# Performance work log

Measured on AMD Instinct MI355X. Metric: run time of the kernel, lower is better.

The kernel has to match this reference:

```python
import jax, jax.numpy as jnp
import numpy as np

B, N, K, DIN, C = 2, 20480, 16, 32, 64  # C = 2*d_out
EPS = 1e-5


def _ln(x, g, b):
    m = jnp.mean(x, axis=-1, keepdims=True)
    v = jnp.mean((x - m) ** 2, axis=-1, keepdims=True)
    return (x - m) * jax.lax.rsqrt(v + EPS) * g + b


def _gather(pc, idx):
    # pc: (B, N, D), idx: (B, N, K) -> (B, N, K, D)
    Bq, Nq, Kq = idx.shape
    D = pc.shape[-1]
    flat = idx.reshape(Bq, Nq * Kq, 1)
    return jnp.take_along_axis(pc, flat, axis=1).reshape(Bq, Nq, Kq, D)


def setup_inputs() -> dict:
    key = jax.random.key(0)
    ks = jax.random.split(key, 40)
    rn = lambda k, s, sc=0.05: jax.random.normal(k, s, dtype=jnp.float32) * sc
    inp = {
        "feature": rn(ks[0], (B, DIN, N, 1), 1.0),
        "xyz": jax.random.uniform(ks[1], (B, N, 3), dtype=jnp.float32),
        "W1": rn(ks[2], (C, DIN)), "b1": rn(ks[3], (C,)),
        "Wq": rn(ks[4], (C, C)), "bq": rn(ks[5], (C,)),
        "Wk": rn(ks[6], (C, C)), "bk": rn(ks[7], (C,)),
        "Wv": rn(ks[8], (C, C)), "bv": rn(ks[9], (C,)),
        "Wd1": rn(ks[10], (3, 3), 0.3), "bd1": rn(ks[11], (3,)),
        "lnd1_g": 1.0 + rn(ks[12], (3,)), "lnd1_b": rn(ks[13], (3,)),
        "Wd2": rn(ks[14], (C, 3), 0.3), "bd2": rn(ks[15], (C,)),
        "Wg1": rn(ks[16], (C, C)), "bg1": rn(ks[17], (C,)),
        "lng1_g": 1.0 + rn(ks[18], (C,)), "lng1_b": rn(ks[19], (C,)),
        "Wg2": rn(ks[20], (C, C)), "bg2": rn(ks[21], (C,)),
        "lng2_g": 1.0 + rn(ks[22], (C,)), "lng2_b": rn(ks[23], (C,)),
        "Wmlp": rn(ks[24], (C, C)),
        "bnm_g": 1.0 + rn(ks[25], (C,)), "bnm_b": rn(ks[26], (C,)),
        "bnm_m": rn(ks[27], (C,)), "bnm_v": 1.0 + jax.random.uniform(ks[28], (C,), dtype=jnp.float32) * 0.1,
        "Wsc": rn(ks[29], (C, DIN)),
        "bns_g": 1.0 + rn(ks[30], (C,)), "bns_b": rn(ks[31], (C,)),
        "bns_m": rn(ks[32], (C,)), "bns_v": 1.0 + jax.random.uniform(ks[33], (C,), dtype=jnp.float32) * 0.1,
        "neigh_idx": jax.random.randint(ks[34], (B, N, K), 0, N),
    }
    return inp


def reference(feature, xyz, W1, b1, Wq, bq, Wk, bk, Wv, bv, Wd1, bd1, lnd1_g, lnd1_b,
              Wd2, bd2, Wg1, bg1, lng1_g, lng1_b, Wg2, bg2, lng2_g, lng2_b,
              Wmlp, bnm_g, bnm_b, bnm_m, bnm_v, Wsc, bns_g, bns_b, bns_m, bns_v,
              neigh_idx):
    f = jnp.transpose(feature[..., 0], (0, 2, 1))          # (B, N, DIN)
    x = f @ W1.T + b1                                      # (B, N, C)
    q = x @ Wq.T + bq                                      # (B, N, C)
    kf = _gather(x @ Wk.T + bk, neigh_idx)                 # (B, N, K, C)
    vf = _gather(x @ Wv.T + bv, neigh_idx)                 # (B, N, K, C)
    knn_xyz = _gather(xyz, neigh_idx)                      # (B, N, K, 3)
    rel = xyz[:, :, None, :] - knn_xyz                     # (B, N, K, 3)
    pos = rel @ Wd1.T + bd1
    pos = jax.nn.relu(_ln(pos, lnd1_g, lnd1_b))
    pos = pos @ Wd2.T + bd2                                # (B, N, K, C)
    attn = q[:, :, None, :] - kf + pos
    attn = jax.nn.relu(_ln(attn, lng1_g, lng1_b)) @ Wg1.T + bg1
    attn = jax.nn.relu(_ln(attn, lng2_g, lng2_b)) @ Wg2.T + bg2
    attn = jax.nn.softmax(attn, axis=2)                    # softmax over K
    res = jnp.sum(attn * (vf + pos), axis=2)               # (B, N, C)
    # mlp: 1x1 conv (no bias) + BN(eval) + ReLU
    res = res @ Wmlp.T
    res = jax.nn.relu(bnm_g * (res - bnm_m) * jax.lax.rsqrt(bnm_v + EPS) + bnm_b)
    # shortcut: 1x1 conv (no bias) + BN(eval) + ReLU
    sc = f @ Wsc.T
    sc = jax.nn.relu(bns_g * (sc - bns_m) * jax.lax.rsqrt(bns_v + EPS) + bns_b)
    out = jax.nn.leaky_relu(res + sc, negative_slope=0.2)  # (B, N, C)
    return jnp.transpose(out, (0, 2, 1))[..., None]        # (B, C, N, 1)
```

## Files before the change

### kernel.cpp

```cpp
#include <hip/hip_runtime.h>

#define N_ 20480
#define EPS_ 1e-5f

typedef __bf16 bf16;
typedef __attribute__((ext_vector_type(8))) __bf16 bf16x8;
typedef __attribute__((ext_vector_type(4))) __bf16 bf16x4;
typedef __attribute__((ext_vector_type(4))) float f32x4;
typedef __attribute__((ext_vector_type(2))) float f32x2;

#define WS_WG1   0
#define WS_WG2   8192
#define WS_PCST  16384
#define WS_L1    17408
#define WS_L2    17920
#define WS_BG1   18432
#define WS_BG2   18688
#define WS_WQ    18944
#define WS_WK    23040
#define WS_WV    27136
#define WS_WSC   31232
#define WS_WMLP  35328
#define WS_BQ    43520
#define WS_BK    43776
#define WS_BV    44032
#define WS_BSC   44288
#define WS_BMLP  44544
#define WS_PD1   44800
#define WS_FLAG  44872
#define WS_PREP  45056

template <typename T>
__device__ __forceinline__ float ldf(const T* p, size_t i) { return (float)p[i]; }

__device__ __forceinline__ int sniff_dtype(const unsigned int* xyz_raw) {
  const int t = threadIdx.x;
  __shared__ int cnt[256];
  int local = 0;
  for (int i = t; i < 4096; i += 256) {
    unsigned int wv = xyz_raw[i];
    unsigned int b1 = (wv >> 8) & 0xFFu;
    local += (b1 >= 0x30u && b1 < 0x45u) ? 1 : 0;
  }
  cnt[t] = local;
  __syncthreads();
  for (int s = 128; s > 0; s >>= 1) {
    if (t < s) cnt[t] += cnt[t + s];
    __syncthreads();
  }
  int r = (cnt[0] > 2048) ? 1 : 0;
  __syncthreads();
  return r;
}

template <typename T>
__device__ void prep_body(const T* W1, const T* b1, const T* Wq, const T* bq,
                          const T* Wk, const T* bk, const T* Wv, const T* bv,
                          const T* Wd1, const T* bd1, const T* lnd1_g, const T* lnd1_b,
                          const T* Wd2, const T* bd2,
                          const T* Wg1, const T* bg1, const T* lng1_g, const T* lng1_b,
                          const T* Wg2, const T* bg2, const T* lng2_g, const T* lng2_b,
                          const T* Wmlp, const T* bnm_g, const T* bnm_b, const T* bnm_m, const T* bnm_v,
                          const T* Wsc, const T* bns_g, const T* bns_b, const T* bns_m, const T* bns_v,
                          char* wsp) {
  const int tid = blockIdx.x * 256 + threadIdx.x;
  const int T_ = gridDim.x * 256;
  bf16* wg1bf = (bf16*)(wsp + WS_WG1);
  bf16* wg2bf = (bf16*)(wsp + WS_WG2);
  bf16* wmlpbf = (bf16*)(wsp + WS_WMLP);
  bf16* wscbf = (bf16*)(wsp + WS_WSC);
  bf16* wqbf = (bf16*)(wsp + WS_WQ);
  bf16* wkbf = (bf16*)(wsp + WS_WK);
  bf16* wvbf = (bf16*)(wsp + WS_WV);
  float* pcst = (float*)(wsp + WS_PCST);
  float* l1c = (float*)(wsp + WS_L1);
  float* l2c = (float*)(wsp + WS_L2);
  float* bg1f = (float*)(wsp + WS_BG1);
  float* bg2f = (float*)(wsp + WS_BG2);
  float* bqf = (float*)(wsp + WS_BQ);
  float* bkf = (float*)(wsp + WS_BK);
  float* bvf = (float*)(wsp + WS_BV);
  float* bscf = (float*)(wsp + WS_BSC);
  float* bmlpf = (float*)(wsp + WS_BMLP);
  float* pd1 = (float*)(wsp + WS_PD1);

  for (int i = tid; i < 4096; i += T_) {
// ... 102 lines not shown

  bf16x8 fa;
  #pragma unroll
  for (int j = 0; j < 8; ++j)
    fa[j] = (__bf16)ldf(feat, ((size_t)b * 32 + g * 8 + j) * N_ + n0 + m);

  auto matmul16 = [&](const bf16* wbf, const float* bias, float* ob) {
    #pragma unroll
    for (int tt = 0; tt < 4; ++tt) {
      bf16x8 wf = *(const bf16x8*)(wbf + (tt * 16 + m) * 32 + g * 8);
      float bb = bias[tt * 16 + m];
      f32x4 ci = {bb, bb, bb, bb};
      ci = __builtin_amdgcn_mfma_f32_16x16x32_bf16(fa, wf, ci, 0, 0, 0);
      #pragma unroll
      for (int r = 0; r < 4; ++r) tw[g * 4 + r][tt * 16 + m] = ci[r];
    }
    #pragma unroll
    for (int s = 0; s < 2; ++s) {
      f32x4 v0 = *(f32x4*)&tw[m][s * 32 + g * 8];
      f32x4 v1 = *(f32x4*)&tw[m][s * 32 + g * 8 + 4];
      #pragma unroll
      for (int r = 0; r < 4; ++r) { ob[s * 8 + r] = v0[r]; ob[s * 8 + 4 + r] = v1[r]; }
    }
  };
  float ob[16];
  bf16x8 o0, o1;
  matmul16(wqbf, bqf, ob);
  #pragma unroll
  for (int j = 0; j < 8; ++j) { o0[j] = (__bf16)ob[j]; o1[j] = (__bf16)ob[8 + j]; }
  *(bf16x8*)(q_ws + (size_t)(p0 + m) * 64 + g * 8) = o0;
  *(bf16x8*)(q_ws + (size_t)(p0 + m) * 64 + 32 + g * 8) = o1;
  matmul16(wkbf, bkf, ob);
  #pragma unroll
  for (int j = 0; j < 8; ++j) { o0[j] = (__bf16)ob[j]; o1[j] = (__bf16)ob[8 + j]; }
  *(bf16x8*)(k_ws + (size_t)(p0 + m) * 64 + g * 8) = o0;
  *(bf16x8*)(k_ws + (size_t)(p0 + m) * 64 + 32 + g * 8) = o1;
  matmul16(wvbf, bvf, ob);
  #pragma unroll
  for (int j = 0; j < 8; ++j) { o0[j] = (__bf16)ob[j]; o1[j] = (__bf16)ob[8 + j]; }
  *(bf16x8*)(v_ws + (size_t)(p0 + m) * 64 + g * 8) = o0;
  *(bf16x8*)(v_ws + (size_t)(p0 + m) * 64 + 32 + g * 8) = o1;
}

__launch_bounds__(256)
__global__ void xqkv_kernel(const void* feat, char* wsp,
                            bf16* q_ws, bf16* k_ws, bf16* v_ws) {
  __shared__ float tile[64][68];
  const int* flag = (const int*)(wsp + WS_FLAG);
  if (flag[0]) xqkv_body<bf16>((const bf16*)feat, wsp, q_ws, k_ws, v_ws, tile);
  else         xqkv_body<float>((const float*)feat, wsp, q_ws, k_ws, v_ws, tile);
}

template <typename T>
__device__ void attn_body(const T* xyz, const int* nidx, const char* wsp,
                          bf16* qres, const bf16* k_ws, const bf16* v_ws,
                          f32x4* pcstL, f32x2* l1L, f32x2* l2L,
                          bf16 (*vpf)[72], bf16 (*scr)[72]) {
  const int t = threadIdx.x;
  ((float*)pcstL)[t] = ((const float*)(wsp + WS_PCST))[t];
  if (t < 128) ((float*)l1L)[t] = ((const float*)(wsp + WS_L1))[t];
  else if (t < 256) ((float*)l2L)[t - 128] = ((const float*)(wsp + WS_L2))[t - 128];
  __syncthreads();

  const int w = t >> 6, lane = t & 63, m = lane & 15, g = lane >> 4;
  const int p = blockIdx.x * 4 + w;
  const int b = p / N_;
  bf16 (*vw)[72] = vpf + w * 16;
  bf16 (*sw)[72] = scr + w * 16;

  const float* pd1 = (const float*)(wsp + WS_PD1);
  const float* bg1f = (const float*)(wsp + WS_BG1);
  const float* bg2f = (const float*)(wsp + WS_BG2);
  const bf16* wg1bf = (const bf16*)(wsp + WS_WG1);
  const bf16* wg2bf = (const bf16*)(wsp + WS_WG2);

  float bg1r[4], bg2r[4];
  #pragma unroll
  for (int tt = 0; tt < 4; ++tt) { bg1r[tt] = bg1f[tt * 16 + m]; bg2r[tt] = bg2f[tt * 16 + m]; }

  float xp = ldf(xyz, (size_t)p * 3 + 0);
  float yp = ldf(xyz, (size_t)p * 3 + 1);
  float zp = ldf(xyz, (size_t)p * 3 + 2);

  int idx = nidx[(size_t)p * 16 + m];
  size_t pg = (size_t)b * N_ + idx;
  bf16x8 kf0 = *(const bf16x8*)(k_ws + pg * 64 + g * 8);
  bf16x8 kf1 = *(const bf16x8*)(k_ws + pg * 64 + 32 + g * 8);
  bf16x8 vf0 = *(const bf16x8*)(v_ws + pg * 64 + g * 8);
  bf16x8 vf1 = *(const bf16x8*)(v_ws + pg * 64 + 32 + g * 8);
  bf16x8 qf0 = *(const bf16x8*)(qres + (size_t)p * 64 + g * 8);
  bf16x8 qf1 = *(const bf16x8*)(qres + (size_t)p * 64 + 32 + g * 8);
  float nx = ldf(xyz, pg * 3 + 0), ny = ldf(xyz, pg * 3 + 1), nz = ldf(xyz, pg * 3 + 2);

  float rx = xp - nx, ry = yp - ny, rz = zp - nz;
  float pp0 = pd1[0] * rx + pd1[1] * ry + pd1[2] * rz + pd1[9];
  float pp1 = pd1[3] * rx + pd1[4] * ry + pd1[5] * rz + pd1[10];
  float pp2 = pd1[6] * rx + pd1[7] * ry + pd1[8] * rz + pd1[11];
  float mu3 = (pp0 + pp1 + pp2) * (1.f / 3.f);
  float q0 = pp0 - mu3, q1 = pp1 - mu3, q2 = pp2 - mu3;
  float vr3 = (q0 * q0 + q1 * q1 + q2 * q2) * (1.f / 3.f);
  float rs3 = rsqrtf(vr3 + EPS_);
  float h0 = fmaxf(q0 * rs3 * pd1[12] + pd1[15], 0.f);
  float h1 = fmaxf(q1 * rs3 * pd1[13] + pd1[16], 0.f);
  float h2 = fmaxf(q2 * rs3 * pd1[14] + pd1[17], 0.f);

  float a[16];
  #pragma unroll
  for (int s = 0; s < 2; ++s)
    #pragma unroll
    for (int half = 0; half < 2; ++half) {
      bf16x4 vb;
      #pragma unroll
      for (int q4 = 0; q4 < 4; ++q4) {
        int j = half * 4 + q4;
        int c = s * 32 + g * 8 + j;
        f32x4 pc = pcstL[c];
        float pos = fmaf(h0, pc[0], fmaf(h1, pc[1], fmaf(h2, pc[2], pc[3])));
        float kv = (float)((s == 0) ? kf0[j] : kf1[j]);
        float vv = (float)((s == 0) ? vf0[j] : vf1[j]);
        float qv = (float)((s == 0) ? qf0[j] : qf1[j]);
        vb[q4] = (__bf16)(vv + pos);
        a[s * 8 + j] = qv - kv + pos;
      }
      *(bf16x4*)&vw[m][s * 32 + g * 8 + half * 4] = vb;
    }

  f32x4 acc[4];
  bf16x8 hf0, hf1;

  {
    float s1 = 0.f, s2 = 0.f;
    #pragma unroll
    for (int i = 0; i < 16; ++i) { s1 += a[i]; s2 = fmaf(a[i], a[i], s2); }
    s1 += __shfl_xor(s1, 16); s2 += __shfl_xor(s2, 16);
    s1 += __shfl_xor(s1, 32); s2 += __shfl_xor(s2, 32);
    float mean = s1 * (1.f / 64.f);
    float var = s2 * (1.f / 64.f) - mean * mean;
    float rsv = rsqrtf(var + EPS_);
    #pragma unroll
    for (int s = 0; s < 2; ++s)
      #pragma unroll
      for (int j = 0; j < 8; ++j) {
        int c = s * 32 + g * 8 + j;
        f32x2 lc = l1L[c];
        float hh = fmaxf(fmaf((a[s * 8 + j] - mean) * rsv, lc[0], lc[1]), 0.f);
        if (s == 0) hf0[j] = (__bf16)hh; else hf1[j] = (__bf16)hh;
      }
  }
  #pragma unroll
  for (int tt = 0; tt < 4; ++tt) {
    bf16x8 w0 = *(const bf16x8*)(wg1bf + (tt * 16 + m) * 64 + g * 8);
    bf16x8 w1 = *(const bf16x8*)(wg1bf + (tt * 16 + m) * 64 + 32 + g * 8);
    f32x4 ci = {bg1r[tt], bg1r[tt], bg1r[tt], bg1r[tt]};
    ci = __builtin_amdgcn_mfma_f32_16x16x32_bf16(hf0, w0, ci, 0, 0, 0);
    ci = __builtin_amdgcn_mfma_f32_16x16x32_bf16(hf1, w1, ci, 0, 0, 0);
    acc[tt] = ci;
  }
  #pragma unroll
  for (int tt = 0; tt < 4; ++tt)
    #pragma unroll
    for (int r = 0; r < 4; ++r)
      sw[g * 4 + r][tt * 16 + m] = (__bf16)acc[tt][r];
  #pragma unroll
  for (int s = 0; s < 2; ++s) {
    bf16x8 av = *(bf16x8*)&sw[m][s * 32 + g * 8];
    #pragma unroll
    for (int j = 0; j < 8; ++j) a[s * 8 + j] = (float)av[j];
  }
  {
    float s1 = 0.f, s2 = 0.f;
    #pragma unroll
    for (int i = 0; i < 16; ++i) { s1 += a[i]; s2 = fmaf(a[i], a[i], s2); }
    s1 += __shfl_xor(s1, 16); s2 += __shfl_xor(s2, 16);
    s1 += __shfl_xor(s1, 32); s2 += __shfl_xor(s2, 32);
    float mean = s1 * (1.f / 64.f);
    float var = s2 * (1.f / 64.f) - mean * mean;
    float rsv = rsqrtf(var + EPS_);
    #pragma unroll
    for (int s = 0; s < 2; ++s)
      #pragma unroll
      for (int j = 0; j < 8; ++j) {
        int c = s * 32 + g * 8 + j;
        f32x2 lc = l2L[c];
        float hh = fmaxf(fmaf((a[s * 8 + j] - mean) * rsv, lc[0], lc[1]), 0.f);
        if (s == 0) hf0[j] = (__bf16)hh; else hf1[j] = (__bf16)hh;
      }
  }
  #pragma unroll
  for (int tt = 0; tt < 4; ++tt) {
    bf16x8 w0 = *(const bf16x8*)(wg2bf + (tt * 16 + m) * 64 + g * 8);
    bf16x8 w1 = *(const bf16x8*)(wg2bf + (tt * 16 + m) * 64 + 32 + g * 8);
    f32x4 ci = {bg2r[tt], bg2r[tt], bg2r[tt], bg2r[tt]};
    ci = __builtin_amdgcn_mfma_f32_16x16x32_bf16(hf0, w0, ci, 0, 0, 0);
    ci = __builtin_amdgcn_mfma_f32_16x16x32_bf16(hf1, w1, ci, 0, 0, 0);
    acc[tt] = ci;
  }
  float resv[4];
  #pragma unroll
  for (int tt = 0; tt < 4; ++tt) {
    f32x4 l = acc[tt];
    float mx = fmaxf(fmaxf(l[0], l[1]), fmaxf(l[2], l[3]));
    mx = fmaxf(mx, __shfl_xor(mx, 16));
    mx = fmaxf(mx, __shfl_xor(mx, 32));
    float x0 = __expf(l[0] - mx), x1 = __expf(l[1] - mx);
    float x2 = __expf(l[2] - mx), x3 = __expf(l[3] - mx);
    float ss = x0 + x1 + x2 + x3;
    ss += __shfl_xor(ss, 16); ss += __shfl_xor(ss, 32);
    int cc = tt * 16 + m;
    float part = x0 * (float)vw[g * 4 + 0][cc] + x1 * (float)vw[g * 4 + 1][cc]
               + x2 * (float)vw[g * 4 + 2][cc] + x3 * (float)vw[g * 4 + 3][cc];
    part += __shfl_xor(part, 16); part += __shfl_xor(part, 32);
    resv[tt] = part / ss;
  }
  float outv = (g == 0) ? resv[0] : (g == 1) ? resv[1] : (g == 2) ? resv[2] : resv[3];
  qres[(size_t)p * 64 + lane] = (__bf16)outv;
}

__launch_bounds__(256)
__global__ void attn_kernel(const void* xyz, const int* __restrict__ nidx, char* wsp,
                            bf16* qres, const bf16* k_ws, const bf16* v_ws) {
  __shared__ f32x4 pcstL[64];
  __shared__ f32x2 l1L[64];
  __shared__ f32x2 l2L[64];
  __shared__ bf16 vpf[64][72];
  __shared__ bf16 scr[64][72];
  const int* flag = (const int*)(wsp + WS_FLAG);
  if (flag[0])
    attn_body<bf16>((const bf16*)xyz, nidx, wsp, qres, k_ws, v_ws, pcstL, l1L, l2L, vpf, scr);
  else
    attn_body<float>((const float*)xyz, nidx, wsp, qres, k_ws, v_ws, pcstL, l1L, l2L, vpf, scr);
}

template <typename T>
__device__ void out_body(const T* feat, const bf16* res_ws, const char* wsp, T* out,
                         float (*tileT)[69]) {
  const int t = threadIdx.x, w = t >> 6, lane = t & 63;
  const int m = lane & 15, g = lane >> 4;
  const int p0blk = blockIdx.x * 64;
  const int b = p0blk / N_, n0 = p0blk % N_;
  const int p0w = p0blk + w * 16;
  const bf16* wmlpbf = (const bf16*)(wsp + WS_WMLP);
  const bf16* wscbf = (const bf16*)(wsp + WS_WSC);
  const float* bmlpf = (const float*)(wsp + WS_BMLP);
  const float* bscf = (const float*)(wsp + WS_BSC);

  bf16x8 ar0 = *(const bf16x8*)(res_ws + (size_t)(p0w + m) * 64 + g * 8);
  bf16x8 ar1 = *(const bf16x8*)(res_ws + (size_t)(p0w + m) * 64 + 32 + g * 8);
  bf16x8 af;
  #pragma unroll
  for (int j = 0; j < 8; ++j)
    af[j] = (__bf16)ldf(feat, ((size_t)b * 32 + g * 8 + j) * N_ + (n0 + w * 16) + m);

  #pragma unroll
  for (int tt = 0; tt < 4; ++tt) {
    bf16x8 wm0 = *(const bf16x8*)(wmlpbf + (tt * 16 + m) * 64 + g * 8);
    bf16x8 wm1 = *(const bf16x8*)(wmlpbf + (tt * 16 + m) * 64 + 32 + g * 8);
    bf16x8 wsf = *(const bf16x8*)(wscbf + (tt * 16 + m) * 32 + g * 8);
    float bm = bmlpf[tt * 16 + m], bs = bscf[tt * 16 + m];
    f32x4 cm = {bm, bm, bm, bm};
    cm = __builtin_amdgcn_mfma_f32_16x16x32_bf16(ar0, wm0, cm, 0, 0, 0);
    cm = __builtin_amdgcn_mfma_f32_16x16x32_bf16(ar1, wm1, cm, 0, 0, 0);
    f32x4 cs = {bs, bs, bs, bs};
    cs = __builtin_amdgcn_mfma_f32_16x16x32_bf16(af, wsf, cs, 0, 0, 0);
    #pragma unroll
    for (int r = 0; r < 4; ++r) {
      float o = fmaxf(cm[r], 0.f) + fmaxf(cs[r], 0.f);
      o = (o > 0.f) ? o : 0.2f * o;
      tileT[tt * 16 + m][w * 16 + g * 4 + r] = o;
    }
  }
  __syncthreads();
  const int ln = t & 63, grp = t >> 6;
  #pragma unroll
  for (int k = 0; k < 16; ++k) {
    int c2 = grp * 16 + k;
    out[((size_t)b * 64 + c2) * N_ + n0 + ln] = (T)tileT[c2][ln];
  }
}

__launch_bounds__(256)
__global__ void out_kernel(const void* feat, const bf16* res_ws, char* wsp, void* out) {
  __shared__ float tileT[64][69];
  const int* flag = (const int*)(wsp + WS_FLAG);
  if (flag[0]) out_body<bf16>((const bf16*)feat, res_ws, wsp, (bf16*)out, tileT);
  else         out_body<float>((const float*)feat, res_ws, wsp, (float*)out, tileT);
}

extern "C" void kernel_launch(void* const* d_in, const int* in_sizes, int n_in,
                              void* d_out, int out_size, void* d_ws, size_t ws_size,
                              hipStream_t stream) {
  const void* feature = d_in[0];
  const void* xyz     = d_in[1];
  const int*  nidx    = (const int*)d_in[34];

  char* ws = (char*)d_ws;
  bf16* q_ws = (bf16*)(ws + WS_PREP);
  bf16* k_ws = (bf16*)(ws + WS_PREP + 5242880);
  bf16* v_ws = (bf16*)(ws + WS_PREP + 10485760);

  prep_kernel<<<64, 256, 0, stream>>>(xyz,
                                      d_in[2], d_in[3], d_in[4], d_in[5], d_in[6], d_in[7],
                                      d_in[8], d_in[9], d_in[10], d_in[11], d_in[12], d_in[13],
                                      d_in[14], d_in[15], d_in[16], d_in[17], d_in[18], d_in[19],
                                      d_in[20], d_in[21], d_in[22], d_in[23], d_in[24], d_in[25],
                                      d_in[26], d_in[27], d_in[28], d_in[29], d_in[30], d_in[31],
                                      d_in[32], d_in[33], ws);
  xqkv_kernel<<<640, 256, 0, stream>>>(feature, ws, q_ws, k_ws, v_ws);
  attn_kernel<<<10240, 256, 0, stream>>>(xyz, nidx, ws, q_ws, k_ws, v_ws);
  out_kernel<<<640, 256, 0, stream>>>(feature, q_ws, ws, d_out);
}
```

Measured before the change: 268.3 us.

## Fuse output MLP and shortcut into attention kernel, 16 points per block

Folds the output projection, shortcut conv, BN-ReLU and leaky ReLU into the attention kernel. Each block now handles 16 points, four per wave over a loop, and keeps the attention result in shared memory. This removes one kernel launch and the workspace round trip of the intermediate result. In exchange there are four times fewer blocks, a serial per-wave loop, and output stores of 4-element chunks instead of fully coalesced 64-wide rows.

```diff
diff --git a/kernel.cpp b/kernel.cpp
--- a/kernel.cpp
+++ b/kernel.cpp
@@ -8,6 +8,7 @@
 typedef __attribute__((ext_vector_type(4))) __bf16 bf16x4;
 typedef __attribute__((ext_vector_type(4))) float f32x4;
 typedef __attribute__((ext_vector_type(2))) float f32x2;
+typedef __attribute__((ext_vector_type(4))) unsigned short u16x4;
 
 #define WS_WG1   0
 #define WS_WG2   8192
@@ -32,6 +33,23 @@
 
 template <typename T>
 __device__ __forceinline__ float ldf(const T* p, size_t i) { return (float)p[i]; }
+
+__device__ __forceinline__ unsigned short f2bfu(float f) {
+  union { __bf16 b; unsigned short u; } cv; cv.b = (__bf16)f; return cv.u;
+}
+
+template <typename T>
+__device__ __forceinline__ void store4(T* p, float a, float b, float c, float d);
+template <>
+__device__ __forceinline__ void store4<bf16>(bf16* p, float a, float b, float c, float d) {
+  u16x4 v = {f2bfu(a), f2bfu(b), f2bfu(c), f2bfu(d)};
+  *(u16x4*)p = v;
+}
+template <>
+__device__ __forceinline__ void store4<float>(float* p, float a, float b, float c, float d) {
+  f32x4 v = {a, b, c, d};
+  *(f32x4*)p = v;
+}
 
 __device__ __forceinline__ int sniff_dtype(const unsigned int* xyz_raw) {
   const int t = threadIdx.x;
@@ -240,10 +258,10 @@
 }
 
 template <typename T>
-__device__ void attn_body(const T* xyz, const int* nidx, const char* wsp,
-                          bf16* qres, const bf16* k_ws, const bf16* v_ws,
+__device__ void attn_body(const T* xyz, const T* feat, const int* nidx, const char* wsp,
+                          const bf16* q_ws, const bf16* k_ws, const bf16* v_ws, T* out,
                           f32x4* pcstL, f32x2* l1L, f32x2* l2L,
-                          bf16 (*vpf)[72], bf16 (*scr)[72]) {
+                          bf16 (*vpf)[72], bf16 (*scr)[72], bf16 (*res_tile)[72]) {
   const int t = threadIdx.x;
   ((float*)pcstL)[t] = ((const float*)(wsp + WS_PCST))[t];
   if (t < 128) ((float*)l1L)[t] = ((const float*)(wsp + WS_L1))[t];
@@ -251,8 +269,8 @@
   __syncthreads();
 
   const int w = t >> 6, lane = t & 63, m = lane & 15, g = lane >> 4;
-  const int p = blockIdx.x * 4 + w;
-  const int b = p / N_;
+  const int p0 = blockIdx.x * 16;
+  const int b = p0 / N_, n0 = p0 % N_;
   bf16 (*vw)[72] = vpf + w * 16;
   bf16 (*sw)[72] = scr + w * 16;
 
@@ -266,212 +284,198 @@
   #pragma unroll
   for (int tt = 0; tt < 4; ++tt) { bg1r[tt] = bg1f[tt * 16 + m]; bg2r[tt] = bg2f[tt * 16 + m]; }
 
-  float xp = ldf(xyz, (size_t)p * 3 + 0);
-  float yp = ldf(xyz, (size_t)p * 3 + 1);
-  float zp = ldf(xyz, (size_t)p * 3 + 2);
-
-  int idx = nidx[(size_t)p * 16 + m];
-  size_t pg = (size_t)b * N_ + idx;
-  bf16x8 kf0 = *(const bf16x8*)(k_ws + pg * 64 + g * 8);
-  bf16x8 kf1 = *(const bf16x8*)(k_ws + pg * 64 + 32 + g * 8);
-  bf16x8 vf0 = *(const bf16x8*)(v_ws + pg * 64 + g * 8);
-  bf16x8 vf1 = *(const bf16x8*)(v_ws + pg * 64 + 32 + g * 8);
-  bf16x8 qf0 = *(const bf16x8*)(qres + (size_t)p * 64 + g * 8);
-  bf16x8 qf1 = *(const bf16x8*)(qres + (size_t)p * 64 + 32 + g * 8);
-  float nx = ldf(xyz, pg * 3 + 0), ny = ldf(xyz, pg * 3 + 1), nz = ldf(xyz, pg * 3 + 2);
-
-  float rx = xp - nx, ry = yp - ny, rz = zp - nz;
-  float pp0 = pd1[0] * rx + pd1[1] * ry + pd1[2] * rz + pd1[9];
-  float pp1 = pd1[3] * rx + pd1[4] * ry + pd1[5] * rz + pd1[10];
-  float pp2 = pd1[6] * rx + pd1[7] * ry + pd1[8] * rz + pd1[11];
-  float mu3 = (pp0 + pp1 + pp2) * (1.f / 3.f);
-  float q0 = pp0 - mu3, q1 = pp1 - mu3, q2 = pp2 - mu3;
-  float vr3 = (q0 * q0 + q1 * q1 + q2 * q2) * (1.f / 3.f);
-  float rs3 = rsqrtf(vr3 + EPS_);
-  float h0 = fmaxf(q0 * rs3 * pd1[12] + pd1[15], 0.f);
-  float h1 = fmaxf(q1 * rs3 * pd1[13] + pd1[16], 0.f);
-  float h2 = fmaxf(q2 * rs3 * pd1[14] + pd1[17], 0.f);
-
-  float a[16];
-  #pragma unroll
-  for (int s = 0; s < 2; ++s)
-    #pragma unroll
-    for (int half = 0; half < 2; ++half) {
-      bf16x4 vb;
-      #pragma unroll
-      for (int q4 = 0; q4 < 4; ++q4) {
-        int j = half * 4 + q4;
-        int c = s * 32 + g * 8 + j;
-        f32x4 pc = pcstL[c];
-        float pos = fmaf(h0, pc[0], fmaf(h1, pc[1], fmaf(h2, pc[2], pc[3])));
-        float kv = (float)((s == 0) ? kf0[j] : kf1[j]);
-        float vv = (float)((s == 0) ? vf0[j] : vf1[j]);
-        float qv = (float)((s == 0) ? qf0[j] : qf1[j]);
-        vb[q4] = (__bf16)(vv + pos);
-        a[s * 8 + j] = qv - kv + pos;
+  bf16x8 af;
+  #pragma unroll
+  for (int j = 0; j < 8; ++j)
+    af[j] = (__bf16)ldf(feat, ((size_t)b * 32 + g * 8 + j) * N_ + n0 + m);
+
+  #pragma unroll 1
+  for (int it = 0; it < 4; ++it) {
+    const int ptl = w * 4 + it;
+    const int p = p0 + ptl;
+
+    float xp = ldf(xyz, (size_t)p * 3 + 0);
+    float yp = ldf(xyz, (size_t)p * 3 + 1);
+    float zp = ldf(xyz, (size_t)p * 3 + 2);
+
+    int idx = nidx[(size_t)p * 16 + m];
+    size_t pg = (size_t)b * N_ + idx;
+    bf16x8 kf0 = *(const bf16x8*)(k_ws + pg * 64 + g * 8);
+    bf16x8 kf1 = *(const bf16x8*)(k_ws + pg * 64 + 32 + g * 8);
+    bf16x8 vf0 = *(const bf16x8*)(v_ws + pg * 64 + g * 8);
+    bf16x8 vf1 = *(const bf16x8*)(v_ws + pg * 64 + 32 + g * 8);
+    bf16x8 qf0 = *(const bf16x8*)(q_ws + (size_t)p * 64 + g * 8);
+    bf16x8 qf1 = *(const bf16x8*)(q_ws + (size_t)p * 64 + 32 + g * 8);
+    float nx = ldf(xyz, pg * 3 + 0), ny = ldf(xyz, pg * 3 + 1), nz = ldf(xyz, pg * 3 + 2);
+
+    float rx = xp - nx, ry = yp - ny, rz = zp - nz;
+    float pp0 = pd1[0] * rx + pd1[1] * ry + pd1[2] * rz + pd1[9];
+    float pp1 = pd1[3] * rx + pd1[4] * ry + pd1[5] * rz + pd1[10];
+    float pp2 = pd1[6] * rx + pd1[7] * ry + pd1[8] * rz + pd1[11];
+    float mu3 = (pp0 + pp1 + pp2) * (1.f / 3.f);
+    float q0 = pp0 - mu3, q1 = pp1 - mu3, q2 = pp2 - mu3;
+    float vr3 = (q0 * q0 + q1 * q1 + q2 * q2) * (1.f / 3.f);
+    float rs3 = rsqrtf(vr3 + EPS_);
+    float h0 = fmaxf(q0 * rs3 * pd1[12] + pd1[15], 0.f);
+    float h1 = fmaxf(q1 * rs3 * pd1[13] + pd1[16], 0.f);
+    float h2 = fmaxf(q2 * rs3 * pd1[14] + pd1[17], 0.f);
+
+    float a[16];
+    #pragma unroll
+    for (int s = 0; s < 2; ++s)
+      #pragma unroll
+      for (int half = 0; half < 2; ++half) {
+        bf16x4 vb;
+        #pragma unroll
+        for (int q4 = 0; q4 < 4; ++q4) {
+          int j = half * 4 + q4;
+          int c = s * 32 + g * 8 + j;
+          f32x4 pc = pcstL[c];
+          float pos = fmaf(h0, pc[0], fmaf(h1, pc[1], fmaf(h2, pc[2], pc[3])));
+          float kv = (float)((s == 0) ? kf0[j] : kf1[j]);
+          float vv = (float)((s == 0) ? vf0[j] : vf1[j]);
+          float qv = (float)((s == 0) ? qf0[j] : qf1[j]);
+          vb[q4] = (__bf16)(vv + pos);
+          a[s * 8 + j] = qv - kv + pos;
+        }
+        *(bf16x4*)&vw[m][s * 32 + g * 8 + half * 4] = vb;
       }
-      *(bf16x4*)&vw[m][s * 32 + g * 8 + half * 4] = vb;
-    }
-
-  f32x4 acc[4];
-  bf16x8 hf0, hf1;
-
-  {
-    float s1 = 0.f, s2 = 0.f;
-    #pragma unroll
-    for (int i = 0; i < 16; ++i) { s1 += a[i]; s2 = fmaf(a[i], a[i], s2); }
-    s1 += __shfl_xor(s1, 16); s2 += __shfl_xor(s2, 16);
-    s1 += __shfl_xor(s1, 32); s2 += __shfl_xor(s2, 32);
-    float mean = s1 * (1.f / 64.f);
-    float var = s2 * (1.f / 64.f) - mean * mean;
-    float rsv = rsqrtf(var + EPS_);
-    #pragma unroll
-    for (int s = 0; s < 2; ++s)
-      #pragma unroll
-      for (int j = 0; j < 8; ++j) {
-        int c = s * 32 + g * 8 + j;
-        f32x2 lc = l1L[c];
-        float hh = fmaxf(fmaf((a[s * 8 + j] - mean) * rsv, lc[0], lc[1]), 0.f);
-        if (s == 0) hf0[j] = (__bf16)hh; else hf1[j] = (__bf16)hh;
-      }
-  }
-  #pragma unroll
-  for (int tt = 0; tt < 4; ++tt) {
-    bf16x8 w0 = *(const bf16x8*)(wg1bf + (tt * 16 + m) * 64 + g * 8);
-    bf16x8 w1 = *(const bf16x8*)(wg1bf + (tt * 16 + m) * 64 + 32 + g * 8);
-    f32x4 ci = {bg1r[tt], bg1r[tt], bg1r[tt], bg1r[tt]};
-    ci = __builtin_amdgcn_mfma_f32_16x16x32_bf16(hf0, w0, ci, 0, 0, 0);
-    ci = __builtin_amdgcn_mfma_f32_16x16x32_bf16(hf1, w1, ci, 0, 0, 0);
-    acc[tt] = ci;
-  }
-  #pragma unroll
-  for (int tt = 0; tt < 4; ++tt)
-    #pragma unroll
-    for (int r = 0; r < 4; ++r)
-      sw[g * 4 + r][tt * 16 + m] = (__bf16)acc[tt][r];
-  #pragma unroll
-  for (int s = 0; s < 2; ++s) {
-    bf16x8 av = *(bf16x8*)&sw[m][s * 32 + g * 8];
-    #pragma unroll
-    for (int j = 0; j < 8; ++j) a[s * 8 + j] = (float)av[j];
-  }
-  {
-    float s1 = 0.f, s2 = 0.f;
-    #pragma unroll
-    for (int i = 0; i < 16; ++i) { s1 += a[i]; s2 = fmaf(a[i], a[i], s2); }
-    s1 += __shfl_xor(s1, 16); s2 += __shfl_xor(s2, 16);
-    s1 += __shfl_xor(s1, 32); s2 += __shfl_xor(s2, 32);
-    float mean = s1 * (1.f / 64.f);
-    float var = s2 * (1.f / 64.f) - mean * mean;
-    float rsv = rsqrtf(var + EPS_);
-    #pragma unroll
-    for (int s = 0; s < 2; ++s)
-      #pragma unroll
-      for (int j = 0; j < 8; ++j) {
-        int c = s * 32 + g * 8 + j;
-        f32x2 lc = l2L[c];
-        float hh = fmaxf(fmaf((a[s * 8 + j] - mean) * rsv, lc[0], lc[1]), 0.f);
-        if (s == 0) hf0[j] = (__bf16)hh; else hf1[j] = (__bf16)hh;
-      }
-  }
-  #pragma unroll
-  for (int tt = 0; tt < 4; ++tt) {
-    bf16x8 w0 = *(const bf16x8*)(wg2bf + (tt * 16 + m) * 64 + g * 8);
-    bf16x8 w1 = *(const bf16x8*)(wg2bf + (tt * 16 + m) * 64 + 32 + g * 8);
-    f32x4 ci = {bg2r[tt], bg2r[tt], bg2r[tt], bg2r[tt]};
-    ci = __builtin_amdgcn_mfma_f32_16x16x32_bf16(hf0, w0, ci, 0, 0, 0);
-    ci = __builtin_amdgcn_mfma_f32_16x16x32_bf16(hf1, w1, ci, 0, 0, 0);
-    acc[tt] = ci;
-  }
-  float resv[4];
-  #pragma unroll
-  for (int tt = 0; tt < 4; ++tt) {
-    f32x4 l = acc[tt];
-    float mx = fmaxf(fmaxf(l[0], l[1]), fmaxf(l[2], l[3]));
-    mx = fmaxf(mx, __shfl_xor(mx, 16));
-    mx = fmaxf(mx, __shfl_xor(mx, 32));
-    float x0 = __expf(l[0] - mx), x1 = __expf(l[1] - mx);
-    float x2 = __expf(l[2] - mx), x3 = __expf(l[3] - mx);
-    float ss = x0 + x1 + x2 + x3;
-    ss += __shfl_xor(ss, 16); ss += __shfl_xor(ss, 32);
-    int cc = tt * 16 + m;
-    float part = x0 * (float)vw[g * 4 + 0][cc] + x1 * (float)vw[g * 4 + 1][cc]
-               + x2 * (float)vw[g * 4 + 2][cc] + x3 * (float)vw[g * 4 + 3][cc];
-    part += __shfl_xor(part, 16); part += __shfl_xor(part, 32);
-    resv[tt] = part / ss;
-  }
-  float outv = (g == 0) ? resv[0] : (g == 1) ? resv[1] : (g == 2) ? resv[2] : resv[3];
-  qres[(size_t)p * 64 + lane] = (__bf16)outv;
+
+    f32x4 acc[4];
+    bf16x8 hf0, hf1;
+
+    {
+      float s1 = 0.f, s2 = 0.f;
+      #pragma unroll
+      for (int i = 0; i < 16; ++i) { s1 += a[i]; s2 = fmaf(a[i], a[i], s2); }
+      s1 += __shfl_xor(s1, 16); s2 += __shfl_xor(s2, 16);
+      s1 += __shfl_xor(s1, 32); s2 += __shfl_xor(s2, 32);
+      float mean = s1 * (1.f / 64.f);
+      float var = s2 * (1.f / 64.f) - mean * mean;
+      float rsv = rsqrtf(var + EPS_);
+      #pragma unroll
+      for (int s = 0; s < 2; ++s)
+        #pragma unroll
+        for (int j = 0; j < 8; ++j) {
+          int c = s * 32 + g * 8 + j;
+          f32x2 lc = l1L[c];
+          float hh = fmaxf(fmaf((a[s * 8 + j] - mean) * rsv, lc[0], lc[1]), 0.f);
+          if (s == 0) hf0[j] = (__bf16)hh; else hf1[j] = (__bf16)hh;
+        }
+    }
+    #pragma unroll
+    for (int tt = 0; tt < 4; ++tt) {
+      bf16x8 w0 = *(const bf16x8*)(wg1bf + (tt * 16 + m) * 64 + g * 8);
+      bf16x8 w1 = *(const bf16x8*)(wg1bf + (tt * 16 + m) * 64 + 32 + g * 8);
+      f32x4 ci = {bg1r[tt], bg1r[tt], bg1r[tt], bg1r[tt]};
+      ci = __builtin_amdgcn_mfma_f32_16x16x32_bf16(hf0, w0, ci, 0, 0, 0);
+      ci = __builtin_amdgcn_mfma_f32_16x16x32_bf16(hf1, w1, ci, 0, 0, 0);
+      acc[tt] = ci;
+    }
+    #pragma unroll
+    for (int tt = 0; tt < 4; ++tt)
+      #pragma unroll
+      for (int r = 0; r < 4; ++r)
+        sw[g * 4 + r][tt * 16 + m] = (__bf16)acc[tt][r];
+    #pragma unroll
+    for (int s = 0; s < 2; ++s) {
+      bf16x8 av = *(bf16x8*)&sw[m][s * 32 + g * 8];
+      #pragma unroll
+      for (int j = 0; j < 8; ++j) a[s * 8 + j] = (float)av[j];
+    }
+    {
+      float s1 = 0.f, s2 = 0.f;
+      #pragma unroll
+      for (int i = 0; i < 16; ++i) { s1 += a[i]; s2 = fmaf(a[i], a[i], s2); }
+      s1 += __shfl_xor(s1, 16); s2 += __shfl_xor(s2, 16);
+      s1 += __shfl_xor(s1, 32); s2 += __shfl_xor(s2, 32);
+      float mean = s1 * (1.f / 64.f);
+      float var = s2 * (1.f / 64.f) - mean * mean;
+      float rsv = rsqrtf(var + EPS_);
+      #pragma unroll
+      for (int s = 0; s < 2; ++s)
+        #pragma unroll
+        for (int j = 0; j < 8; ++j) {
+          int c = s * 32 + g * 8 + j;
+          f32x2 lc = l2L[c];
+          float hh = fmaxf(fmaf((a[s * 8 + j] - mean) * rsv, lc[0], lc[1]), 0.f);
+          if (s == 0) hf0[j] = (__bf16)hh; else hf1[j] = (__bf16)hh;
+        }
+    }
+    #pragma unroll
+    for (int tt = 0; tt < 4; ++tt) {
+      bf16x8 w0 = *(const bf16x8*)(wg2bf + (tt * 16 + m) * 64 + g * 8);
+      bf16x8 w1 = *(const bf16x8*)(wg2bf + (tt * 16 + m) * 64 + 32 + g * 8);
+      f32x4 ci = {bg2r[tt], bg2r[tt], bg2r[tt], bg2r[tt]};
+      ci = __builtin_amdgcn_mfma_f32_16x16x32_bf16(hf0, w0, ci, 0, 0, 0);
+      ci = __builtin_amdgcn_mfma_f32_16x16x32_bf16(hf1, w1, ci, 0, 0, 0);
+      acc[tt] = ci;
+    }
+    float resv[4];
+    #pragma unroll
+    for (int tt = 0; tt < 4; ++tt) {
+      f32x4 l = acc[tt];
+      float mx = fmaxf(fmaxf(l[0], l[1]), fmaxf(l[2], l[3]));
+      mx = fmaxf(mx, __shfl_xor(mx, 16));
+      mx = fmaxf(mx, __shfl_xor(mx, 32));
+      float x0 = __expf(l[0] - mx), x1 = __expf(l[1] - mx);
+      float x2 = __expf(l[2] - mx), x3 = __expf(l[3] - mx);
+      float ss = x0 + x1 + x2 + x3;
+      ss += __shfl_xor(ss, 16); ss += __shfl_xor(ss, 32);
+      int cc = tt * 16 + m;
+      float part = x0 * (float)vw[g * 4 + 0][cc] + x1 * (float)vw[g * 4 + 1][cc]
+                 + x2 * (float)vw[g * 4 + 2][cc] + x3 * (float)vw[g * 4 + 3][cc];
+      part += __shfl_xor(part, 16); part += __shfl_xor(part, 32);
+      resv[tt] = part / ss;
+    }
+    float outv = (g == 0) ? resv[0] : (g == 1) ? resv[1] : (g == 2) ? resv[2] : resv[3];
+    res_tile[ptl][lane] = (__bf16)outv;
+  }
+
+  __syncthreads();
+
+  const bf16* wmlpbf = (const bf16*)(wsp + WS_WMLP);
+  const bf16* wscbf = (const bf16*)(wsp + WS_WSC);
+  const float* bmlpf = (const float*)(wsp + WS_BMLP);
+  const float* bscf = (const float*)(wsp + WS_BSC);
+
+  bf16x8 ar0 = *(const bf16x8*)&res_tile[m][g * 8];
+  bf16x8 ar1 = *(const bf16x8*)&res_tile[m][32 + g * 8];
+  bf16x8 wm0 = *(const bf16x8*)(wmlpbf + (w * 16 + m) * 64 + g * 8);
+  bf16x8 wm1 = *(const bf16x8*)(wmlpbf + (w * 16 + m) * 64 + 32 + g * 8);
+  bf16x8 wsf = *(const bf16x8*)(wscbf + (w * 16 + m) * 32 + g * 8);
+  float bm = bmlpf[w * 16 + m], bs = bscf[w * 16 + m];
+  f32x4 cm = {bm, bm, bm, bm};
+  cm = __builtin_amdgcn_mfma_f32_16x16x32_bf16(ar0, wm0, cm, 0, 0, 0);
+  cm = __builtin_amdgcn_mfma_f32_16x16x32_bf16(ar1, wm1, cm, 0, 0, 0);
+  f32x4 cs = {bs, bs, bs, bs};
+  cs = __builtin_amdgcn_mfma_f32_16x16x32_bf16(af, wsf, cs, 0, 0, 0);
+  float o[4];
+  #pragma unroll
+  for (int r = 0; r < 4; ++r) {
+    float v = fmaxf(cm[r], 0.f) + fmaxf(cs[r], 0.f);
+    o[r] = (v > 0.f) ? v : 0.2f * v;
+  }
+  store4(out + ((size_t)b * 64 + w * 16 + m) * N_ + n0 + g * 4, o[0], o[1], o[2], o[3]);
 }
 
 __launch_bounds__(256)
-__global__ void attn_kernel(const void* xyz, const int* __restrict__ nidx, char* wsp,
-                            bf16* qres, const bf16* k_ws, const bf16* v_ws) {
+__global__ void attn_kernel(const void* xyz, const void* feat, const int* __restrict__ nidx,
+                            char* wsp, const bf16* q_ws, const bf16* k_ws, const bf16* v_ws,
+                            void* out) {
   __shared__ f32x4 pcstL[64];
   __shared__ f32x2 l1L[64];
   __shared__ f32x2 l2L[64];
   __shared__ bf16 vpf[64][72];
   __shared__ bf16 scr[64][72];
+  __shared__ bf16 res_tile[16][72];
   const int* flag = (const int*)(wsp + WS_FLAG);
   if (flag[0])
-    attn_body<bf16>((const bf16*)xyz, nidx, wsp, qres, k_ws, v_ws, pcstL, l1L, l2L, vpf, scr);
+    attn_body<bf16>((const bf16*)xyz, (const bf16*)feat, nidx, wsp, q_ws, k_ws, v_ws,
+                    (bf16*)out, pcstL, l1L, l2L, vpf, scr, res_tile);
   else
-    attn_body<float>((const float*)xyz, nidx, wsp, qres, k_ws, v_ws, pcstL, l1L, l2L, vpf, scr);
-}
-
-template <typename T>
-__device__ void out_body(const T* feat, const bf16* res_ws, const char* wsp, T* out,
-                         float (*tileT)[69]) {
-  const int t = threadIdx.x, w = t >> 6, lane = t & 63;
-  const int m = lane & 15, g = lane >> 4;
-  const int p0blk = blockIdx.x * 64;
-  const int b = p0blk / N_, n0 = p0blk % N_;
-  const int p0w = p0blk + w * 16;
-  const bf16* wmlpbf = (const bf16*)(wsp + WS_WMLP);
-  const bf16* wscbf = (const bf16*)(wsp + WS_WSC);
-  const float* bmlpf = (const float*)(wsp + WS_BMLP);
-  const float* bscf = (const float*)(wsp + WS_BSC);
-
-  bf16x8 ar0 = *(const bf16x8*)(res_ws + (size_t)(p0w + m) * 64 + g * 8);
-  bf16x8 ar1 = *(const bf16x8*)(res_ws + (size_t)(p0w + m) * 64 + 32 + g * 8);
-  bf16x8 af;
-  #pragma unroll
-  for (int j = 0; j < 8; ++j)
-    af[j] = (__bf16)ldf(feat, ((size_t)b * 32 + g * 8 + j) * N_ + (n0 + w * 16) + m);
-
-  #pragma unroll
-  for (int tt = 0; tt < 4; ++tt) {
-    bf16x8 wm0 = *(const bf16x8*)(wmlpbf + (tt * 16 + m) * 64 + g * 8);
-    bf16x8 wm1 = *(const bf16x8*)(wmlpbf + (tt * 16 + m) * 64 + 32 + g * 8);
-    bf16x8 wsf = *(const bf16x8*)(wscbf + (tt * 16 + m) * 32 + g * 8);
-    float bm = bmlpf[tt * 16 + m], bs = bscf[tt * 16 + m];
-    f32x4 cm = {bm, bm, bm, bm};
-    cm = __builtin_amdgcn_mfma_f32_16x16x32_bf16(ar0, wm0, cm, 0, 0, 0);
-    cm = __builtin_amdgcn_mfma_f32_16x16x32_bf16(ar1, wm1, cm, 0, 0, 0);
-    f32x4 cs = {bs, bs, bs, bs};
-    cs = __builtin_amdgcn_mfma_f32_16x16x32_bf16(af, wsf, cs, 0, 0, 0);
-    #pragma unroll
-    for (int r = 0; r < 4; ++r) {
-      float o = fmaxf(cm[r], 0.f) + fmaxf(cs[r], 0.f);
-      o = (o > 0.f) ? o : 0.2f * o;
-      tileT[tt * 16 + m][w * 16 + g * 4 + r] = o;
-    }
-  }
-  __syncthreads();
-  const int ln = t & 63, grp = t >> 6;
-  #pragma unroll
-  for (int k = 0; k < 16; ++k) {
-    int c2 = grp * 16 + k;
-    out[((size_t)b * 64 + c2) * N_ + n0 + ln] = (T)tileT[c2][ln];
-  }
-}
-
-__launch_bounds__(256)
-__global__ void out_kernel(const void* feat, const bf16* res_ws, char* wsp, void* out) {
-  __shared__ float tileT[64][69];
-  const int* flag = (const int*)(wsp + WS_FLAG);
-  if (flag[0]) out_body<bf16>((const bf16*)feat, res_ws, wsp, (bf16*)out, tileT);
-  else         out_body<float>((const float*)feat, res_ws, wsp, (float*)out, tileT);
+    attn_body<float>((const float*)xyz, (const float*)feat, nidx, wsp, q_ws, k_ws, v_ws,
+                     (float*)out, pcstL, l1L, l2L, vpf, scr, res_tile);
 }
 
 extern "C" void kernel_launch(void* const* d_in, const int* in_sizes, int n_in,
@@ -494,6 +498,5 @@
                                       d_in[26], d_in[27], d_in[28], d_in[29], d_in[30], d_in[31],
                                       d_in[32], d_in[33], ws);
   xqkv_kernel<<<640, 256, 0, stream>>>(feature, ws, q_ws, k_ws, v_ws);
-  attn_kernel<<<10240, 256, 0, stream>>>(xyz, nidx, ws, q_ws, k_ws, v_ws);
-  out_kernel<<<640, 256, 0, stream>>>(feature, q_ws, ws, d_out);
-}
+  attn_kernel<<<2560, 256, 0, stream>>>(xyz, feature, nidx, ws, q_ws, k_ws, v_ws, d_out);
+}
```

After: 315.5 us. 17.6% more time.

## Process two points per wavefront in attention kernel to reuse weight fragments

Applied to the files above, without the earlier changes.

Each wavefront now handles two query points instead of one, so the Wg1/Wg2 weight fragments loaded per tile are shared by two sets of MFMAs. The two points' gathers and MFMAs are interleaved, which gives more independent work per wave to hide latency. The grid is halved and LDS scratch doubled. In exchange, register pressure and LDS use per block rise, which may lower occupancy.

```diff
diff --git a/kernel.cpp b/kernel.cpp
--- a/kernel.cpp
+++ b/kernel.cpp
@@ -251,10 +251,7 @@
   __syncthreads();
 
   const int w = t >> 6, lane = t & 63, m = lane & 15, g = lane >> 4;
-  const int p = blockIdx.x * 4 + w;
-  const int b = p / N_;
-  bf16 (*vw)[72] = vpf + w * 16;
-  bf16 (*sw)[72] = scr + w * 16;
+  const int pbase = blockIdx.x * 8 + w * 2;
 
   const float* pd1 = (const float*)(wsp + WS_PD1);
   const float* bg1f = (const float*)(wsp + WS_BG1);
@@ -266,60 +263,69 @@
   #pragma unroll
   for (int tt = 0; tt < 4; ++tt) { bg1r[tt] = bg1f[tt * 16 + m]; bg2r[tt] = bg2f[tt * 16 + m]; }
 
-  float xp = ldf(xyz, (size_t)p * 3 + 0);
-  float yp = ldf(xyz, (size_t)p * 3 + 1);
-  float zp = ldf(xyz, (size_t)p * 3 + 2);
-
-  int idx = nidx[(size_t)p * 16 + m];
-  size_t pg = (size_t)b * N_ + idx;
-  bf16x8 kf0 = *(const bf16x8*)(k_ws + pg * 64 + g * 8);
-  bf16x8 kf1 = *(const bf16x8*)(k_ws + pg * 64 + 32 + g * 8);
-  bf16x8 vf0 = *(const bf16x8*)(v_ws + pg * 64 + g * 8);
-  bf16x8 vf1 = *(const bf16x8*)(v_ws + pg * 64 + 32 + g * 8);
-  bf16x8 qf0 = *(const bf16x8*)(qres + (size_t)p * 64 + g * 8);
-  bf16x8 qf1 = *(const bf16x8*)(qres + (size_t)p * 64 + 32 + g * 8);
-  float nx = ldf(xyz, pg * 3 + 0), ny = ldf(xyz, pg * 3 + 1), nz = ldf(xyz, pg * 3 + 2);
-
-  float rx = xp - nx, ry = yp - ny, rz = zp - nz;
-  float pp0 = pd1[0] * rx + pd1[1] * ry + pd1[2] * rz + pd1[9];
-  float pp1 = pd1[3] * rx + pd1[4] * ry + pd1[5] * rz + pd1[10];
-  float pp2 = pd1[6] * rx + pd1[7] * ry + pd1[8] * rz + pd1[11];
-  float mu3 = (pp0 + pp1 + pp2) * (1.f / 3.f);
-  float q0 = pp0 - mu3, q1 = pp1 - mu3, q2 = pp2 - mu3;
-  float vr3 = (q0 * q0 + q1 * q1 + q2 * q2) * (1.f / 3.f);
-  float rs3 = rsqrtf(vr3 + EPS_);
-  float h0 = fmaxf(q0 * rs3 * pd1[12] + pd1[15], 0.f);
-  float h1 = fmaxf(q1 * rs3 * pd1[13] + pd1[16], 0.f);
-  float h2 = fmaxf(q2 * rs3 * pd1[14] + pd1[17], 0.f);
-
-  float a[16];
-  #pragma unroll
-  for (int s = 0; s < 2; ++s)
-    #pragma unroll
-    for (int half = 0; half < 2; ++half) {
-      bf16x4 vb;
-      #pragma unroll
-      for (int q4 = 0; q4 < 4; ++q4) {
-        int j = half * 4 + q4;
-        int c = s * 32 + g * 8 + j;
-        f32x4 pc = pcstL[c];
-        float pos = fmaf(h0, pc[0], fmaf(h1, pc[1], fmaf(h2, pc[2], pc[3])));
-        float kv = (float)((s == 0) ? kf0[j] : kf1[j]);
-        float vv = (float)((s == 0) ? vf0[j] : vf1[j]);
-        float qv = (float)((s == 0) ? qf0[j] : qf1[j]);
-        vb[q4] = (__bf16)(vv + pos);
-        a[s * 8 + j] = qv - kv + pos;
+  float a[2][16];
+
+  #pragma unroll
+  for (int P = 0; P < 2; ++P) {
+    const int p = pbase + P;
+    const int b = p / N_;
+    bf16 (*vw)[72] = vpf + (w * 2 + P) * 16;
+
+    float xp = ldf(xyz, (size_t)p * 3 + 0);
+    float yp = ldf(xyz, (size_t)p * 3 + 1);
+    float zp = ldf(xyz, (size_t)p * 3 + 2);
+
+    int idx = nidx[(size_t)p * 16 + m];
+    size_t pg = (size_t)b * N_ + idx;
+    bf16x8 kf0 = *(const bf16x8*)(k_ws + pg * 64 + g * 8);
+    bf16x8 kf1 = *(const bf16x8*)(k_ws + pg * 64 + 32 + g * 8);
+    bf16x8 vf0 = *(const bf16x8*)(v_ws + pg * 64 + g * 8);
+    bf16x8 vf1 = *(const bf16x8*)(v_ws + pg * 64 + 32 + g * 8);
+    bf16x8 qf0 = *(const bf16x8*)(qres + (size_t)p * 64 + g * 8);
+    bf16x8 qf1 = *(const bf16x8*)(qres + (size_t)p * 64 + 32 + g * 8);
+    float nx = ldf(xyz, pg * 3 + 0), ny = ldf(xyz, pg * 3 + 1), nz = ldf(xyz, pg * 3 + 2);
+
+    float rx = xp - nx, ry = yp - ny, rz = zp - nz;
+    float pp0 = pd1[0] * rx + pd1[1] * ry + pd1[2] * rz + pd1[9];
+    float pp1 = pd1[3] * rx + pd1[4] * ry + pd1[5] * rz + pd1[10];
+    float pp2 = pd1[6] * rx + pd1[7] * ry + pd1[8] * rz + pd1[11];
+    float mu3 = (pp0 + pp1 + pp2) * (1.f / 3.f);
+    float q0 = pp0 - mu3, q1 = pp1 - mu3, q2 = pp2 - mu3;
+    float vr3 = (q0 * q0 + q1 * q1 + q2 * q2) * (1.f / 3.f);
+    float rs3 = rsqrtf(vr3 + EPS_);
+    float h0 = fmaxf(q0 * rs3 * pd1[12] + pd1[15], 0.f);
+    float h1 = fmaxf(q1 * rs3 * pd1[13] + pd1[16], 0.f);
+    float h2 = fmaxf(q2 * rs3 * pd1[14] + pd1[17], 0.f);
+
+    #pragma unroll
+    for (int s = 0; s < 2; ++s)
+      #pragma unroll
+      for (int half = 0; half < 2; ++half) {
+        bf16x4 vb;
+        #pragma unroll
+        for (int q4 = 0; q4 < 4; ++q4) {
+          int j = half * 4 + q4;
+          int c = s * 32 + g * 8 + j;
+          f32x4 pc = pcstL[c];
+          float pos = fmaf(h0, pc[0], fmaf(h1, pc[1], fmaf(h2, pc[2], pc[3])));
+          float kv = (float)((s == 0) ? kf0[j] : kf1[j]);
+          float vv = (float)((s == 0) ? vf0[j] : vf1[j]);
+          float qv = (float)((s == 0) ? qf0[j] : qf1[j]);
+          vb[q4] = (__bf16)(vv + pos);
+          a[P][s * 8 + j] = qv - kv + pos;
+        }
+        *(bf16x4*)&vw[m][s * 32 + g * 8 + half * 4] = vb;
       }
-      *(bf16x4*)&vw[m][s * 32 + g * 8 + half * 4] = vb;
-    }
-
-  f32x4 acc[4];
-  bf16x8 hf0, hf1;
-
-  {
+  }
+
+  bf16x8 hf0[2], hf1[2];
+  f32x4 acc[2][4];
+
+  #pragma unroll
+  for (int P = 0; P < 2; ++P) {
     float s1 = 0.f, s2 = 0.f;
     #pragma unroll
-    for (int i = 0; i < 16; ++i) { s1 += a[i]; s2 = fmaf(a[i], a[i], s2); }
+    for (int i = 0; i < 16; ++i) { s1 += a[P][i]; s2 = fmaf(a[P][i], a[P][i], s2); }
     s1 += __shfl_xor(s1, 16); s2 += __shfl_xor(s2, 16);
     s1 += __shfl_xor(s1, 32); s2 += __shfl_xor(s2, 32);
     float mean = s1 * (1.f / 64.f);
@@ -331,34 +337,46 @@
       for (int j = 0; j < 8; ++j) {
         int c = s * 32 + g * 8 + j;
         f32x2 lc = l1L[c];
-        float hh = fmaxf(fmaf((a[s * 8 + j] - mean) * rsv, lc[0], lc[1]), 0.f);
-        if (s == 0) hf0[j] = (__bf16)hh; else hf1[j] = (__bf16)hh;
+        float hh = fmaxf(fmaf((a[P][s * 8 + j] - mean) * rsv, lc[0], lc[1]), 0.f);
+        if (s == 0) hf0[P][j] = (__bf16)hh; else hf1[P][j] = (__bf16)hh;
       }
   }
   #pragma unroll
   for (int tt = 0; tt < 4; ++tt) {
     bf16x8 w0 = *(const bf16x8*)(wg1bf + (tt * 16 + m) * 64 + g * 8);
     bf16x8 w1 = *(const bf16x8*)(wg1bf + (tt * 16 + m) * 64 + 32 + g * 8);
-    f32x4 ci = {bg1r[tt], bg1r[tt], bg1r[tt], bg1r[tt]};
-    ci = __builtin_amdgcn_mfma_f32_16x16x32_bf16(hf0, w0, ci, 0, 0, 0);
-    ci = __builtin_amdgcn_mfma_f32_16x16x32_bf16(hf1, w1, ci, 0, 0, 0);
-    acc[tt] = ci;
-  }
-  #pragma unroll
-  for (int tt = 0; tt < 4; ++tt)
-    #pragma unroll
-    for (int r = 0; r < 4; ++r)
-      sw[g * 4 + r][tt * 16 + m] = (__bf16)acc[tt][r];
-  #pragma unroll
-  for (int s = 0; s < 2; ++s) {
-    bf16x8 av = *(bf16x8*)&sw[m][s * 32 + g * 8];
-    #pragma unroll
-    for (int j = 0; j < 8; ++j) a[s * 8 + j] = (float)av[j];
-  }
-  {
+    #pragma unroll
+    for (int P = 0; P < 2; ++P) {
+      f32x4 ci = {bg1r[tt], bg1r[tt], bg1r[tt], bg1r[tt]};
+      ci = __builtin_amdgcn_mfma_f32_16x16x32_bf16(hf0[P], w0, ci, 0, 0, 0);
+      ci = __builtin_amdgcn_mfma_f32_16x16x32_bf16(hf1[P], w1, ci, 0, 0, 0);
+      acc[P][tt] = ci;
+    }
+  }
+  #pragma unroll
+  for (int P = 0; P < 2; ++P) {
+    bf16 (*sw)[72] = scr + (w * 2 + P) * 16;
+    #pragma unroll
+    for (int tt = 0; tt < 4; ++tt)
+      #pragma unroll
+      for (int r = 0; r < 4; ++r)
+        sw[g * 4 + r][tt * 16 + m] = (__bf16)acc[P][tt][r];
+  }
+  #pragma unroll
+  for (int P = 0; P < 2; ++P) {
+    bf16 (*sw)[72] = scr + (w * 2 + P) * 16;
+    #pragma unroll
+    for (int s = 0; s < 2; ++s) {
+      bf16x8 av = *(bf16x8*)&sw[m][s * 32 + g * 8];
+      #pragma unroll
+      for (int j = 0; j < 8; ++j) a[P][s * 8 + j] = (float)av[j];
+    }
+  }
+  #pragma unroll
+  for (int P = 0; P < 2; ++P) {
     float s1 = 0.f, s2 = 0.f;
     #pragma unroll
-    for (int i = 0; i < 16; ++i) { s1 += a[i]; s2 = fmaf(a[i], a[i], s2); }
+    for (int i = 0; i < 16; ++i) { s1 += a[P][i]; s2 = fmaf(a[P][i], a[P][i], s2); }
     s1 += __shfl_xor(s1, 16); s2 += __shfl_xor(s2, 16);
     s1 += __shfl_xor(s1, 32); s2 += __shfl_xor(s2, 32);
     float mean = s1 * (1.f / 64.f);
@@ -370,38 +388,46 @@
       for (int j = 0; j < 8; ++j) {
         int c = s * 32 + g * 8 + j;
         f32x2 lc = l2L[c];
-        float hh = fmaxf(fmaf((a[s * 8 + j] - mean) * rsv, lc[0], lc[1]), 0.f);
-        if (s == 0) hf0[j] = (__bf16)hh; else hf1[j] = (__bf16)hh;
+        float hh = fmaxf(fmaf((a[P][s * 8 + j] - mean) * rsv, lc[0], lc[1]), 0.f);
+        if (s == 0) hf0[P][j] = (__bf16)hh; else hf1[P][j] = (__bf16)hh;
       }
   }
   #pragma unroll
   for (int tt = 0; tt < 4; ++tt) {
     bf16x8 w0 = *(const bf16x8*)(wg2bf + (tt * 16 + m) * 64 + g * 8);
     bf16x8 w1 = *(const bf16x8*)(wg2bf + (tt * 16 + m) * 64 + 32 + g * 8);
-    f32x4 ci = {bg2r[tt], bg2r[tt], bg2r[tt], bg2r[tt]};
-    ci = __builtin_amdgcn_mfma_f32_16x16x32_bf16(hf0, w0, ci, 0, 0, 0);
-    ci = __builtin_amdgcn_mfma_f32_16x16x32_bf16(hf1, w1, ci, 0, 0, 0);
-    acc[tt] = ci;
-  }
-  float resv[4];
-  #pragma unroll
-  for (int tt = 0; tt < 4; ++tt) {
-    f32x4 l = acc[tt];
-    float mx = fmaxf(fmaxf(l[0], l[1]), fmaxf(l[2], l[3]));
-    mx = fmaxf(mx, __shfl_xor(mx, 16));
-    mx = fmaxf(mx, __shfl_xor(mx, 32));
-    float x0 = __expf(l[0] - mx), x1 = __expf(l[1] - mx);
-    float x2 = __expf(l[2] - mx), x3 = __expf(l[3] - mx);
-    float ss = x0 + x1 + x2 + x3;
-    ss += __shfl_xor(ss, 16); ss += __shfl_xor(ss, 32);
-    int cc = tt * 16 + m;
-    float part = x0 * (float)vw[g * 4 + 0][cc] + x1 * (float)vw[g * 4 + 1][cc]
-               + x2 * (float)vw[g * 4 + 2][cc] + x3 * (float)vw[g * 4 + 3][cc];
-    part += __shfl_xor(part, 16); part += __shfl_xor(part, 32);
-    resv[tt] = part / ss;
-  }
-  float outv = (g == 0) ? resv[0] : (g == 1) ? resv[1] : (g == 2) ? resv[2] : resv[3];
-  qres[(size_t)p * 64 + lane] = (__bf16)outv;
+    #pragma unroll
+    for (int P = 0; P < 2; ++P) {
+      f32x4 ci = {bg2r[tt], bg2r[tt], bg2r[tt], bg2r[tt]};
+      ci = __builtin_amdgcn_mfma_f32_16x16x32_bf16(hf0[P], w0, ci, 0, 0, 0);
+      ci = __builtin_amdgcn_mfma_f32_16x16x32_bf16(hf1[P], w1, ci, 0, 0, 0);
+      acc[P][tt] = ci;
+    }
+  }
+  #pragma unroll
+  for (int P = 0; P < 2; ++P) {
+    const int p = pbase + P;
+    bf16 (*vw)[72] = vpf + (w * 2 + P) * 16;
+    float resv[4];
+    #pragma unroll
+    for (int tt = 0; tt < 4; ++tt) {
+      f32x4 l = acc[P][tt];
+      float mx = fmaxf(fmaxf(l[0], l[1]), fmaxf(l[2], l[3]));
+      mx = fmaxf(mx, __shfl_xor(mx, 16));
+      mx = fmaxf(mx, __shfl_xor(mx, 32));
+      float x0 = __expf(l[0] - mx), x1 = __expf(l[1] - mx);
+      float x2 = __expf(l[2] - mx), x3 = __expf(l[3] - mx);
+      float ss = x0 + x1 + x2 + x3;
+      ss += __shfl_xor(ss, 16); ss += __shfl_xor(ss, 32);
+      int cc = tt * 16 + m;
+      float part = x0 * (float)vw[g * 4 + 0][cc] + x1 * (float)vw[g * 4 + 1][cc]
+                 + x2 * (float)vw[g * 4 + 2][cc] + x3 * (float)vw[g * 4 + 3][cc];
+      part += __shfl_xor(part, 16); part += __shfl_xor(part, 32);
+      resv[tt] = part / ss;
+    }
+    float outv = (g == 0) ? resv[0] : (g == 1) ? resv[1] : (g == 2) ? resv[2] : resv[3];
+    qres[(size_t)p * 64 + lane] = (__bf16)outv;
+  }
 }
 
 __launch_bounds__(256)
@@ -410,8 +436,8 @@
   __shared__ f32x4 pcstL[64];
   __shared__ f32x2 l1L[64];
   __shared__ f32x2 l2L[64];
-  __shared__ bf16 vpf[64][72];
-  __shared__ bf16 scr[64][72];
+  __shared__ bf16 vpf[128][72];
+  __shared__ bf16 scr[128][72];
   const int* flag = (const int*)(wsp + WS_FLAG);
   if (flag[0])
     attn_body<bf16>((const bf16*)xyz, nidx, wsp, qres, k_ws, v_ws, pcstL, l1L, l2L, vpf, scr);
@@ -494,6 +520,6 @@
                                       d_in[26], d_in[27], d_in[28], d_in[29], d_in[30], d_in[31],
                                       d_in[32], d_in[33], ws);
   xqkv_kernel<<<640, 256, 0, stream>>>(feature, ws, q_ws, k_ws, v_ws);
-  attn_kernel<<<10240, 256, 0, stream>>>(xyz, nidx, ws, q_ws, k_ws, v_ws);
+  attn_kernel<<<5120, 256, 0, stream>>>(xyz, nidx, ws, q_ws, k_ws, v_ws);
   out_kernel<<<640, 256, 0, stream>>>(feature, q_ws, ws, d_out);
 }
```

After: 241.3 us. 10.1% less time.
